# Optimization experiments

Measured on AMD Instinct MI355X. Metric: run time of the kernel, lower is better.

The kernel has to match this reference:

```python
import jax, jax.numpy as jnp
import numpy as np

HIDDEN = 2048
NUM_HEADS = 16
NUM_KV_HEADS = 16
QK_NOPE = 128
QK_ROPE = 64
HEAD_DIM = QK_NOPE + QK_ROPE  # 192
V_HEAD = 128
KV_LORA = 512
Q_LORA = 1536
EPS = 1e-6


def rmsnorm(x, w):
    var = jnp.mean(x * x, axis=-1, keepdims=True)
    return x * jax.lax.rsqrt(var + EPS) * w


def setup_inputs() -> dict:
    key = jax.random.key(0)
    ks = jax.random.split(key, 8)
    s = lambda fan_in: 1.0 / np.sqrt(fan_in)
    return {
        "hidden_states": jax.random.normal(ks[0], (2, 2048, HIDDEN), jnp.float32),
        # weights stored as [in, out] so forward is x @ W
        "q_a_w": jax.random.normal(ks[1], (HIDDEN, Q_LORA), jnp.float32) * s(HIDDEN),
        "q_a_ln_w": jnp.ones((Q_LORA,), jnp.float32),
        "q_b_w": jax.random.normal(ks[2], (Q_LORA, NUM_HEADS * HEAD_DIM), jnp.float32) * s(Q_LORA),
        "kv_a_w": jax.random.normal(ks[3], (HIDDEN, KV_LORA + NUM_KV_HEADS * QK_ROPE), jnp.float32) * s(HIDDEN),
        "kv_a_ln_w": jnp.ones((KV_LORA,), jnp.float32),
        "kv_b_w": jax.random.normal(ks[4], (KV_LORA, NUM_KV_HEADS * (QK_NOPE + V_HEAD)), jnp.float32) * s(KV_LORA),
        "o_w": jax.random.normal(ks[5], (NUM_HEADS * V_HEAD, HIDDEN), jnp.float32) * s(NUM_HEADS * V_HEAD),
    }


def reference(hidden_states, q_a_w, q_a_ln_w, q_b_w, kv_a_w, kv_a_ln_w, kv_b_w, o_w):
    B, T, _ = hidden_states.shape
    # Q path: low-rank down-proj -> RMSNorm -> up-proj
    q = rmsnorm(hidden_states @ q_a_w, q_a_ln_w) @ q_b_w
    q = q.reshape(B, T, NUM_HEADS, HEAD_DIM)  # [B,T,H,192]

    # KV path: joint down-proj producing latent + rope slice
    kv_raw = hidden_states @ kv_a_w
    kv_latent = rmsnorm(kv_raw[..., :KV_LORA], kv_a_ln_w)
    k_rope = kv_raw[..., KV_LORA:].reshape(B, T, NUM_KV_HEADS, QK_ROPE)
    kv = (kv_latent @ kv_b_w).reshape(B, T, NUM_KV_HEADS, QK_NOPE + V_HEAD)
    k_nope = kv[..., :QK_NOPE]
    v = kv[..., QK_NOPE:]  # [B,T,Hkv,128]

    # NOTE: the original forward computes RoPE cos/sin but never applies the
    # rotation; q_rope/k_rope are used as-is (faithfully reproduced here).
    k = jnp.concatenate([k_nope, k_rope], axis=-1)  # [B,T,Hkv,192]
    # num_kv_groups == 1, so no repeat_interleave needed

    scale = 1.0 / jnp.sqrt(jnp.float32(HEAD_DIM))
    scores = jnp.einsum("bqhd,bkhd->bhqk", q, k) * scale  # [B,H,T,T]
    causal = jnp.tril(jnp.ones((T, T), bool))
    scores = jnp.where(causal, scores, jnp.finfo(scores.dtype).min)
    probs = jax.nn.softmax(scores, axis=-1)
    attn = jnp.einsum("bhqk,bkhd->bqhd", probs, v)  # [B,T,H,128]
    attn = attn.reshape(B, T, NUM_HEADS * V_HEAD)
    return attn @ o_w
```

## Files before the change

### kernel.cpp

```cpp
#include <hip/hip_runtime.h>
#include <cstdint>
#include <cstddef>

typedef unsigned short u16;
typedef short short8 __attribute__((ext_vector_type(8)));
typedef float f32x4 __attribute__((ext_vector_type(4)));

#define B_   2
#define T_   2048
#define H_   16
#define HID_ 2048
#define DQK_ 192
#define DV_  128
#define AW_  3072

__device__ __forceinline__ float bf2f(u16 u) {
  unsigned int v = ((unsigned int)u) << 16;
  return __builtin_bit_cast(float, v);
}
__device__ __forceinline__ u16 f2bf(float f) {
  unsigned int u = __builtin_bit_cast(unsigned int, f);
  u += 0x7fff + ((u >> 16) & 1);
  return (u16)(u >> 16);
}
__device__ __forceinline__ void load_lds16(const void* g, void* l) {
  __builtin_amdgcn_global_load_lds((const __attribute__((address_space(1))) void*)g,
                                   (__attribute__((address_space(3))) void*)l, 16, 0, 0);
}

__global__ __launch_bounds__(256) void cast_f32_bf16(const float* __restrict__ x,
                                                     u16* __restrict__ y) {
  size_t i = ((size_t)blockIdx.x * 256 + threadIdx.x) * 8;
  float4 a = *(const float4*)&x[i];
  float4 b = *(const float4*)&x[i + 4];
  u16 r[8];
  r[0] = f2bf(a.x); r[1] = f2bf(a.y); r[2] = f2bf(a.z); r[3] = f2bf(a.w);
  r[4] = f2bf(b.x); r[5] = f2bf(b.y); r[6] = f2bf(b.z); r[7] = f2bf(b.w);
  *(uint4*)&y[i] = *(const uint4*)&r[0];
}

__global__ __launch_bounds__(256) void transpose_cast_k(const float* __restrict__ W,
                                                        u16* __restrict__ Wt,
                                                        int K, int N) {
  __shared__ u16 tile[32][33];
  int n0 = blockIdx.x * 32, k0 = blockIdx.y * 32;
  int tx = threadIdx.x & 31, ty = threadIdx.x >> 5;
#pragma unroll
  for (int i = 0; i < 32; i += 8)
    tile[ty + i][tx] = f2bf(W[(size_t)(k0 + ty + i) * N + n0 + tx]);
  __syncthreads();
#pragma unroll
  for (int i = 0; i < 32; i += 8)
    Wt[(size_t)(n0 + ty + i) * K + k0 + tx] = tile[tx][ty + i];
}

__global__ __launch_bounds__(256) void rmsnorm_k(const u16* __restrict__ in, int in_stride,
                                                 int L, const float* __restrict__ w,
                                                 u16* __restrict__ out, int out_stride) {
  int row = blockIdx.x;
  const u16* x = in + (size_t)row * in_stride;
  float ss = 0.f;
  for (int i = threadIdx.x * 8; i < L; i += 2048) {
    uint4 v = *(const uint4*)&x[i];
    const u16* p = (const u16*)&v;
#pragma unroll
    for (int e = 0; e < 8; ++e) { float f = bf2f(p[e]); ss += f * f; }
  }
#pragma unroll
  for (int m = 32; m >= 1; m >>= 1) ss += __shfl_xor(ss, m);
  __shared__ float red[4];
  if ((threadIdx.x & 63) == 0) red[threadIdx.x >> 6] = ss;
  __syncthreads();
  ss = red[0] + red[1] + red[2] + red[3];
  float inv = rsqrtf(ss / (float)L + 1e-6f);
  u16* o = out + (size_t)row * out_stride;
  for (int i = threadIdx.x * 8; i < L; i += 2048) {
    uint4 v = *(const uint4*)&x[i];
    const u16* p = (const u16*)&v;
    u16 r8[8];
#pragma unroll
    for (int e = 0; e < 8; ++e) r8[e] = f2bf(bf2f(p[e]) * inv * w[i + e]);
    *(uint4*)&o[i] = *(const uint4*)&r8[0];
  }
}

template <int EPI>
__global__ __launch_bounds__(256) void gemm_bt(const u16* __restrict__ A,
                                               const u16* __restrict__ Bt,
                                               void* __restrict__ Cout,
                                               int M, int N, int K) {
  __shared__ u16 As[3][128 * 32];
  __shared__ u16 Bs[3][128 * 32];
  const int nbx = N >> 7;
  const int bx = blockIdx.x % nbx, by = blockIdx.x / nbx;
  const int m0 = by << 7, n0 = bx << 7;
  const int tid = threadIdx.x, w = tid >> 6, lane = tid & 63;
  const int wr = w >> 1, wc = w & 1;
  const int llo = lane & 15, lhi = lane >> 4;
  f32x4 acc[4][4] = {};

  const int c0 = tid, c1 = tid + 256;
  const int ar0 = c0 >> 2, s0_ = c0 & 3;
  const int ar1 = c1 >> 2, s1_ = c1 & 3;
  const u16* Asrc0 = A + (size_t)(m0 + ar0) * K + (s0_ ^ ((ar0 >> 1) & 3)) * 8;
  const u16* Asrc1 = A + (size_t)(m0 + ar1) * K + (s1_ ^ ((ar1 >> 1) & 3)) * 8;
  const u16* Bsrc0 = Bt + (size_t)(n0 + ar0) * K + (s0_ ^ ((ar0 >> 1) & 3)) * 8;
  const u16* Bsrc1 = Bt + (size_t)(n0 + ar1) * K + (s1_ ^ ((ar1 >> 1) & 3)) * 8;

  int aoff[4], boff[4];
#pragma unroll
  for (int i = 0; i < 4; ++i) {
    int rowa = wr * 64 + i * 16 + llo;
    aoff[i] = (rowa * 4 + (lhi ^ ((rowa >> 1) & 3))) * 8;
    int rowb = wc * 64 + i * 16 + llo;
    boff[i] = (rowb * 4 + (lhi ^ ((rowb >> 1) & 3))) * 8;
  }

#define STAGE_KT(kt, buf)                                   \
  do {                                                      \
    int k0_ = (kt) << 5;                                    \
    load_lds16(Asrc0 + k0_, &As[(buf)][c0 * 8]);            \
    load_lds16(Asrc1 + k0_, &As[(buf)][c1 * 8]);            \
    load_lds16(Bsrc0 + k0_, &Bs[(buf)][c0 * 8]);            \
    load_lds16(Bsrc1 + k0_, &Bs[(buf)][c1 * 8]);            \
  } while (0)

  const int NT = K >> 5;
  STAGE_KT(0, 0);
  STAGE_KT(1, 1);
  asm volatile("s_waitcnt vmcnt(4)" ::: "memory");
  __builtin_amdgcn_s_barrier();

  int cur = 0, nxt = 2;
  for (int kt = 0; kt < NT; ++kt) {
    if (kt + 2 < NT) STAGE_KT(kt + 2, nxt);
    short8 af[4], bfr[4];
#pragma unroll
    for (int i = 0; i < 4; ++i) af[i] = *(const short8*)&As[cur][aoff[i]];
#pragma unroll
    for (int j = 0; j < 4; ++j) bfr[j] = *(const short8*)&Bs[cur][boff[j]];
    __builtin_amdgcn_s_setprio(1);
#pragma unroll
    for (int i = 0; i < 4; ++i)
#pragma unroll
      for (int j = 0; j < 4; ++j)
        acc[i][j] = __builtin_amdgcn_mfma_f32_16x16x32_bf16(af[i], bfr[j], acc[i][j], 0, 0, 0);
    __builtin_amdgcn_s_setprio(0);
    if (kt + 2 < NT) asm volatile("s_waitcnt vmcnt(4)" ::: "memory");
    else             asm volatile("s_waitcnt vmcnt(0)" ::: "memory");
    __builtin_amdgcn_s_barrier();
    cur = (cur == 2) ? 0 : cur + 1;
    nxt = (nxt == 2) ? 0 : nxt + 1;
  }
#undef STAGE_KT

  if constexpr (EPI == 0) {
    float* C = (float*)Cout;
#pragma unroll
    for (int i = 0; i < 4; ++i)
#pragma unroll
      for (int j = 0; j < 4; ++j)
#pragma unroll
        for (int r = 0; r < 4; ++r)
          C[(size_t)(m0 + wr * 64 + i * 16 + lhi * 4 + r) * N + (n0 + wc * 64 + j * 16 + llo)] =
              acc[i][j][r];
  } else {
    const float scale = (EPI == 3) ? 0.10412163f : 1.0f;
    u16* C = (u16*)Cout;
#pragma unroll
    for (int i = 0; i < 4; ++i)
#pragma unroll
      for (int j = 0; j < 4; ++j)
#pragma unroll
        for (int r = 0; r < 4; ++r)
          C[(size_t)(m0 + wr * 64 + i * 16 + lhi * 4 + r) * N + (n0 + wc * 64 + j * 16 + llo)] =
              f2bf(acc[i][j][r] * scale);
  }
}

__global__ __launch_bounds__(256) void pack_vt_k(const u16* __restrict__ kv, u16* __restrict__ Vt) {
  __shared__ u16 tile[64][136];
  const int nt = T_ / 64;
  int t0 = (blockIdx.x % nt) * 64;
  int bh = blockIdx.x / nt;
  int b = bh >> 4, h = bh & 15;
  int row = threadIdx.x >> 4;
  int ck = threadIdx.x & 15;
#pragma unroll
  for (int i = 0; i < 64; i += 16) {
    uint4 v = *(const uint4*)&kv[((size_t)(b * T_) + t0 + row + i) * 4096 + h * 256 + 128 + ck * 8];
    *(uint4*)&tile[row + i][ck * 8] = v;
  }
  __syncthreads();
  int d = threadIdx.x >> 1;
  int th = (threadIdx.x & 1) * 32;
  u16 tmp[32];
#pragma unroll
  for (int e = 0; e < 32; ++e) tmp[e] = tile[th + e][d];
#pragma unroll
  for (int e = 0; e < 32; e += 8)
    *(uint4*)&Vt[((size_t)bh * 128 + d) * T_ + t0 + th + e] = *(const uint4*)&tmp[e];
}

__global__ __launch_bounds__(256, 2) void attn_k(const u16* __restrict__ q,
                                                 const u16* __restrict__ kv,
                                                 const u16* __restrict__ kvraw,
                                                 const u16* __restrict__ Vt,
                                                 u16* __restrict__ att) {
  constexpr int KLD = 192, VLD = 64, PLD = 64;
  __shared__ u16 Ks[2][64 * KLD];
  __shared__ u16 Vs[128 * VLD];
  __shared__ u16 Ps[64 * PLD];
  const int p = (int)blockIdx.x;
  const int xcd = p & 7, j = p >> 3;
  const int bh = xcd * 4 + (j & 3);
  const int pr = j >> 2;
  const int b = bh >> 4, h = bh & 15;
  const int bT = b * T_;
  const int tid = threadIdx.x, w = tid >> 6, lane = tid & 63;
  const int llo = lane & 15, lhi = lane >> 4;
  const u16* Vb = Vt + (size_t)bh * DV_ * T_;

  const u16* kbase[6]; int kstr[6];
#pragma unroll
  for (int ii = 0; ii < 6; ++ii) {
    int c = ii * 256 + tid;
    int rr = c / 24, chk = c - rr * 24;
    int sc = chk ^ (rr & 7);
    if (sc < 16) { kbase[ii] = kv + (size_t)(bT + rr) * 4096 + h * 256 + sc * 8; kstr[ii] = 4096; }
    else { kbase[ii] = kvraw + (size_t)(bT + rr) * AW_ + 2048 + h * 64 + (sc - 16) * 8; kstr[ii] = AW_; }
  }
  int voff[4];
#pragma unroll
  for (int ii = 0; ii < 4; ++ii) {
    int c = ii * 256 + tid;
    int rr = c >> 3, chk = c & 7;
    voff[ii] = rr * T_ + (chk ^ (rr & 7)) * 8;
  }

#pragma unroll
  for (int pass = 0; pass < 2; ++pass) {
    const int qt = pass == 0 ? 31 - pr : pr;
    const int q0 = qt * 64;
    const int rbase = q0 + w * 16;
    short8 qf[6];
#pragma unroll
    for (int kk = 0; kk < 6; ++kk)
      qf[kk] = *(const short8*)&q[(size_t)(bT + rbase + llo) * AW_ + h * DQK_ + kk * 32 + lhi * 8];
    f32x4 oacc[8] = {};
    float m_r[4], l_r[4];
#pragma unroll
    for (int r = 0; r < 4; ++r) { m_r[r] = -1e30f; l_r[r] = 0.f; }

#pragma unroll
    for (int ii = 0; ii < 6; ++ii)
      load_lds16(kbase[ii], &Ks[0][(ii * 256 + tid) * 8]);
    asm volatile("s_waitcnt vmcnt(0)" ::: "memory");
    __builtin_amdgcn_s_barrier();
    __builtin_amdgcn_sched_barrier(0);

    const int nkt = qt + 1;
    int cur = 0;
    for (int kt = 0; kt < nkt; ++kt) {
      const int k0 = kt * 64;
      const bool hasNext = (kt + 1 < nkt);
#pragma unroll
      for (int ii = 0; ii < 4; ++ii)
        load_lds16(Vb + k0 + voff[ii], &Vs[(ii * 256 + tid) * 8]);
      if (hasNext) {
        u16* kd = Ks[cur ^ 1];
#pragma unroll
        for (int ii = 0; ii < 6; ++ii)
          load_lds16(kbase[ii] + (size_t)(k0 + 64) * kstr[ii], &kd[(ii * 256 + tid) * 8]);
      }
      const u16* kbuf = Ks[cur];
      f32x4 s[4] = {};
      __builtin_amdgcn_s_setprio(1);
#pragma unroll
      for (int kk = 0; kk < 6; ++kk) {
        const int col = kk * 32 + lhi * 8;
        short8 kf[4];
#pragma unroll
        for (int j2 = 0; j2 < 4; ++j2) {
          const int row = j2 * 16 + llo;
          kf[j2] = *(const short8*)&kbuf[row * KLD + (col ^ ((row & 7) << 3))];
        }
#pragma unroll
        for (int j2 = 0; j2 < 4; ++j2)
          s[j2] = __builtin_amdgcn_mfma_f32_16x16x32_bf16(qf[kk], kf[j2], s[j2], 0, 0, 0);
      }
      __builtin_amdgcn_s_setprio(0);
      const bool needMask = (k0 + 63 > rbase);
#pragma unroll
      for (int r = 0; r < 4; ++r) {
        const int qrow = rbase + lhi * 4 + r;
        float sv[4];
#pragma unroll
        for (int j2 = 0; j2 < 4; ++j2) {
          float x = s[j2][r];
          if (needMask) { int kcol = k0 + j2 * 16 + llo; x = (kcol <= qrow) ? x : -1e30f; }
          sv[j2] = x;
        }
        float mx4 = fmaxf(fmaxf(sv[0], sv[1]), fmaxf(sv[2], sv[3]));
        if (!__all(mx4 - m_r[r] <= 8.f)) {
          float mx = mx4;
#pragma unroll
          for (int mk = 1; mk < 16; mk <<= 1) mx = fmaxf(mx, __shfl_xor(mx, mk));
          float mnew = fmaxf(m_r[r], mx);
          float alpha = exp2f(m_r[r] - mnew);
          m_r[r] = mnew;
          l_r[r] *= alpha;
#pragma unroll
          for (int jo = 0; jo < 8; ++jo) oacc[jo][r] *= alpha;
        }
        float rs = 0.f;
        const int prow = w * 16 + lhi * 4 + r;
#pragma unroll
        for (int j2 = 0; j2 < 4; ++j2) {
          float p2 = exp2f(sv[j2] - m_r[r]);
          rs += p2;
          int pcol = j2 * 16 + llo;
          Ps[prow * PLD + (pcol ^ ((prow & 7) << 3))] = f2bf(p2);
        }
        l_r[r] += rs;
      }
      if (hasNext) asm volatile("s_waitcnt vmcnt(6)" ::: "memory");
      else         asm volatile("s_waitcnt vmcnt(0)" ::: "memory");
      __builtin_amdgcn_s_barrier();
      __builtin_amdgcn_sched_barrier(0);
      __builtin_amdgcn_s_setprio(1);
#pragma unroll
      for (int kk2 = 0; kk2 < 2; ++kk2) {
        const int prow = w * 16 + llo;
        const int pcol = kk2 * 32 + lhi * 8;
        short8 pf = *(const short8*)&Ps[prow * PLD + (pcol ^ ((prow & 7) << 3))];
#pragma unroll
        for (int jo = 0; jo < 8; ++jo) {
          const int vrow = jo * 16 + llo;
          short8 vf = *(const short8*)&Vs[vrow * VLD + (pcol ^ ((vrow & 7) << 3))];
          oacc[jo] = __builtin_amdgcn_mfma_f32_16x16x32_bf16(pf, vf, oacc[jo], 0, 0, 0);
        }
      }
      __builtin_amdgcn_s_setprio(0);
      asm volatile("s_waitcnt vmcnt(0)" ::: "memory");
      __builtin_amdgcn_s_barrier();
      __builtin_amdgcn_sched_barrier(0);
      cur ^= 1;
    }
#pragma unroll
    for (int r = 0; r < 4; ++r) {
      float lr = l_r[r];
#pragma unroll
      for (int mk = 1; mk < 16; mk <<= 1) lr += __shfl_xor(lr, mk);
      const int qrow = rbase + lhi * 4 + r;
      const float linv = 1.f / lr;
#pragma unroll
      for (int jo = 0; jo < 8; ++jo)
        att[((size_t)bT + qrow) * (H_ * DV_) + h * DV_ + jo * 16 + llo] =
            f2bf(oacc[jo][r] * linv);
    }
  }
}

extern "C" void kernel_launch(void* const* d_in, const int* in_sizes, int n_in,
                              void* d_out, int out_size, void* d_ws, size_t ws_size,
                              hipStream_t stream) {
  const float* hs      = (const float*)d_in[0];
  const float* q_a_w   = (const float*)d_in[1];
  const float* q_a_ln  = (const float*)d_in[2];
  const float* q_b_w   = (const float*)d_in[3];
  const float* kv_a_w  = (const float*)d_in[4];
  const float* kv_a_ln = (const float*)d_in[5];
  const float* kv_b_w  = (const float*)d_in[6];
  const float* o_w     = (const float*)d_in[7];
  float* out = (float*)d_out;
  char* ws = (char*)d_ws;

  u16* hid  = (u16*)(ws + 0);
  u16* wt   = (u16*)(ws + 16777216);
  u16* qa   = (u16*)(ws + 29360128);
  u16* qan  = (u16*)(ws + 54525952);
  u16* qout = (u16*)(ws + 67108864);
  u16* att  = (u16*)(ws + 92274688);
  u16* kv   = (u16*)(ws + 109051904);
  u16* Vt   = (u16*)(ws + 142606336);

  cast_f32_bf16<<<4096, 256, 0, stream>>>(hs, hid);

  transpose_cast_k<<<dim3(1536 / 32, 2048 / 32), 256, 0, stream>>>(q_a_w, wt, 2048, 1536);
  transpose_cast_k<<<dim3(1536 / 32, 2048 / 32), 256, 0, stream>>>(kv_a_w, wt + (size_t)1536 * 2048, 2048, 1536);
  gemm_bt<1><<<(3072 / 128) * (4096 / 128), 256, 0, stream>>>(hid, wt, qa, 4096, 3072, 2048);

  rmsnorm_k<<<4096, 256, 0, stream>>>(qa, AW_, 1536, q_a_ln, qan, 1536);

  transpose_cast_k<<<dim3(3072 / 32, 1536 / 32), 256, 0, stream>>>(q_b_w, wt, 1536, 3072);
  gemm_bt<3><<<(3072 / 128) * (4096 / 128), 256, 0, stream>>>(qan, wt, qout, 4096, 3072, 1536);

  rmsnorm_k<<<4096, 256, 0, stream>>>(qa + 1536, AW_, 512, kv_a_ln, qan, 512);

  transpose_cast_k<<<dim3(4096 / 32, 512 / 32), 256, 0, stream>>>(kv_b_w, wt, 512, 4096);
  gemm_bt<1><<<(4096 / 128) * (4096 / 128), 256, 0, stream>>>(qan, wt, kv, 4096, 4096, 512);

  pack_vt_k<<<1024, 256, 0, stream>>>(kv, Vt);

  attn_k<<<512, 256, 0, stream>>>(qout, kv, qa, Vt, att);

  transpose_cast_k<<<dim3(2048 / 32, 2048 / 32), 256, 0, stream>>>(o_w, wt, 2048, 2048);
  gemm_bt<0><<<(2048 / 128) * (4096 / 128), 256, 0, stream>>>(att, wt, out, 4096, 2048, 2048);
}
```

Before: 336.4 us.

## Use 32-key tiles, double-buffer V, and one query tile per block

The attention kernel now gives each block a single 64-row query tile, launched as 1024 blocks in heaviest-first order, instead of pairing a heavy and a light tile per block. K tiles shrink to 32 keys and V is double-buffered alongside K, which removes one barrier per iteration. LDS use drops enough to allow three blocks per CU. The aim is better overlap of loads with MFMA work and higher occupancy. The cost is more loop iterations with less MFMA work each, and losing the explicit causal load pairing.

```diff
diff --git a/kernel.cpp b/kernel.cpp
--- a/kernel.cpp
+++ b/kernel.cpp
@@ -202,163 +202,159 @@
     *(uint4*)&Vt[((size_t)bh * 128 + d) * T_ + t0 + th + e] = *(const uint4*)&tmp[e];
 }
 
-__global__ __launch_bounds__(256, 2) void attn_k(const u16* __restrict__ q,
+__global__ __launch_bounds__(256, 3) void attn_k(const u16* __restrict__ q,
                                                  const u16* __restrict__ kv,
                                                  const u16* __restrict__ kvraw,
                                                  const u16* __restrict__ Vt,
                                                  u16* __restrict__ att) {
-  constexpr int KLD = 192, VLD = 64, PLD = 64;
-  __shared__ u16 Ks[2][64 * KLD];
-  __shared__ u16 Vs[128 * VLD];
+  constexpr int KLD = 192;
+  constexpr int VLD = 32;
+  constexpr int PLD = 32;
+  __shared__ u16 Ks[2][32 * KLD];
+  __shared__ u16 Vs[2][128 * VLD];
   __shared__ u16 Ps[64 * PLD];
   const int p = (int)blockIdx.x;
   const int xcd = p & 7, j = p >> 3;
   const int bh = xcd * 4 + (j & 3);
-  const int pr = j >> 2;
+  const int qt = 31 - (j >> 2);
   const int b = bh >> 4, h = bh & 15;
   const int bT = b * T_;
+  const int q0 = qt * 64;
   const int tid = threadIdx.x, w = tid >> 6, lane = tid & 63;
   const int llo = lane & 15, lhi = lane >> 4;
+  const int rbase = q0 + w * 16;
   const u16* Vb = Vt + (size_t)bh * DV_ * T_;
 
-  const u16* kbase[6]; int kstr[6];
-#pragma unroll
-  for (int ii = 0; ii < 6; ++ii) {
+  const u16* kbase[3]; int kstr[3];
+#pragma unroll
+  for (int ii = 0; ii < 3; ++ii) {
     int c = ii * 256 + tid;
     int rr = c / 24, chk = c - rr * 24;
     int sc = chk ^ (rr & 7);
     if (sc < 16) { kbase[ii] = kv + (size_t)(bT + rr) * 4096 + h * 256 + sc * 8; kstr[ii] = 4096; }
     else { kbase[ii] = kvraw + (size_t)(bT + rr) * AW_ + 2048 + h * 64 + (sc - 16) * 8; kstr[ii] = AW_; }
   }
-  int voff[4];
-#pragma unroll
-  for (int ii = 0; ii < 4; ++ii) {
+  const u16* vsrc[2];
+#pragma unroll
+  for (int ii = 0; ii < 2; ++ii) {
     int c = ii * 256 + tid;
-    int rr = c >> 3, chk = c & 7;
-    voff[ii] = rr * T_ + (chk ^ (rr & 7)) * 8;
-  }
-
-#pragma unroll
-  for (int pass = 0; pass < 2; ++pass) {
-    const int qt = pass == 0 ? 31 - pr : pr;
-    const int q0 = qt * 64;
-    const int rbase = q0 + w * 16;
-    short8 qf[6];
-#pragma unroll
-    for (int kk = 0; kk < 6; ++kk)
-      qf[kk] = *(const short8*)&q[(size_t)(bT + rbase + llo) * AW_ + h * DQK_ + kk * 32 + lhi * 8];
-    f32x4 oacc[8] = {};
-    float m_r[4], l_r[4];
-#pragma unroll
-    for (int r = 0; r < 4; ++r) { m_r[r] = -1e30f; l_r[r] = 0.f; }
-
-#pragma unroll
-    for (int ii = 0; ii < 6; ++ii)
-      load_lds16(kbase[ii], &Ks[0][(ii * 256 + tid) * 8]);
+    int rr = c >> 2, sl = c & 3;
+    vsrc[ii] = Vb + (size_t)rr * T_ + (sl ^ (rr & 3)) * 8;
+  }
+
+  short8 qf[6];
+#pragma unroll
+  for (int kk = 0; kk < 6; ++kk)
+    qf[kk] = *(const short8*)&q[(size_t)(bT + rbase + llo) * AW_ + h * DQK_ + kk * 32 + lhi * 8];
+  f32x4 oacc[8] = {};
+  float m_r[4], l_r[4];
+#pragma unroll
+  for (int r = 0; r < 4; ++r) { m_r[r] = -1e30f; l_r[r] = 0.f; }
+
+#pragma unroll
+  for (int ii = 0; ii < 3; ++ii)
+    load_lds16(kbase[ii], &Ks[0][(ii * 256 + tid) * 8]);
+#pragma unroll
+  for (int ii = 0; ii < 2; ++ii)
+    load_lds16(vsrc[ii], &Vs[0][(ii * 256 + tid) * 8]);
+  asm volatile("s_waitcnt vmcnt(0)" ::: "memory");
+  __builtin_amdgcn_s_barrier();
+  __builtin_amdgcn_sched_barrier(0);
+
+  const int nkt = 2 * qt + 2;
+  int cur = 0;
+  for (int kt = 0; kt < nkt; ++kt) {
+    const int k0 = kt * 32;
+    if (kt + 1 < nkt) {
+      u16* kd = Ks[cur ^ 1];
+      u16* vd = Vs[cur ^ 1];
+#pragma unroll
+      for (int ii = 0; ii < 3; ++ii)
+        load_lds16(kbase[ii] + (size_t)(k0 + 32) * kstr[ii], &kd[(ii * 256 + tid) * 8]);
+#pragma unroll
+      for (int ii = 0; ii < 2; ++ii)
+        load_lds16(vsrc[ii] + k0 + 32, &vd[(ii * 256 + tid) * 8]);
+    }
+    const u16* kbuf = Ks[cur];
+    f32x4 s[2] = {};
+    __builtin_amdgcn_s_setprio(1);
+#pragma unroll
+    for (int kk = 0; kk < 6; ++kk) {
+      const int col = kk * 32 + lhi * 8;
+      short8 kf[2];
+#pragma unroll
+      for (int j2 = 0; j2 < 2; ++j2) {
+        const int row = j2 * 16 + llo;
+        kf[j2] = *(const short8*)&kbuf[row * KLD + (col ^ ((row & 7) << 3))];
+      }
+#pragma unroll
+      for (int j2 = 0; j2 < 2; ++j2)
+        s[j2] = __builtin_amdgcn_mfma_f32_16x16x32_bf16(qf[kk], kf[j2], s[j2], 0, 0, 0);
+    }
+    __builtin_amdgcn_s_setprio(0);
+    const bool needMask = (k0 + 31 > rbase);
+#pragma unroll
+    for (int r = 0; r < 4; ++r) {
+      const int qrow = rbase + lhi * 4 + r;
+      float sv[2];
+#pragma unroll
+      for (int j2 = 0; j2 < 2; ++j2) {
+        float x = s[j2][r];
+        if (needMask) { int kcol = k0 + j2 * 16 + llo; x = (kcol <= qrow) ? x : -1e30f; }
+        sv[j2] = x;
+      }
+      float mx2 = fmaxf(sv[0], sv[1]);
+      if (!__all(mx2 - m_r[r] <= 8.f)) {
+        float mx = mx2;
+#pragma unroll
+        for (int mk = 1; mk < 16; mk <<= 1) mx = fmaxf(mx, __shfl_xor(mx, mk));
+        float mnew = fmaxf(m_r[r], mx);
+        float alpha = exp2f(m_r[r] - mnew);
+        m_r[r] = mnew;
+        l_r[r] *= alpha;
+#pragma unroll
+        for (int jo = 0; jo < 8; ++jo) oacc[jo][r] *= alpha;
+      }
+      const int prow = w * 16 + lhi * 4 + r;
+      float rs = 0.f;
+#pragma unroll
+      for (int j2 = 0; j2 < 2; ++j2) {
+        float pv = exp2f(sv[j2] - m_r[r]);
+        rs += pv;
+        int pcol = j2 * 16 + llo;
+        int slot = pcol >> 3;
+        Ps[prow * PLD + ((slot ^ (prow & 3)) * 8) + (pcol & 7)] = f2bf(pv);
+      }
+      l_r[r] += rs;
+    }
+    __builtin_amdgcn_s_setprio(1);
+    {
+      const int prow = w * 16 + llo;
+      short8 pf = *(const short8*)&Ps[prow * PLD + ((lhi ^ (prow & 3)) * 8)];
+#pragma unroll
+      for (int jo = 0; jo < 8; ++jo) {
+        const int vrow = jo * 16 + llo;
+        short8 vf = *(const short8*)&Vs[cur][vrow * VLD + ((lhi ^ (vrow & 3)) * 8)];
+        oacc[jo] = __builtin_amdgcn_mfma_f32_16x16x32_bf16(pf, vf, oacc[jo], 0, 0, 0);
+      }
+    }
+    __builtin_amdgcn_s_setprio(0);
     asm volatile("s_waitcnt vmcnt(0)" ::: "memory");
     __builtin_amdgcn_s_barrier();
     __builtin_amdgcn_sched_barrier(0);
-
-    const int nkt = qt + 1;
-    int cur = 0;
-    for (int kt = 0; kt < nkt; ++kt) {
-      const int k0 = kt * 64;
-      const bool hasNext = (kt + 1 < nkt);
-#pragma unroll
-      for (int ii = 0; ii < 4; ++ii)
-        load_lds16(Vb + k0 + voff[ii], &Vs[(ii * 256 + tid) * 8]);
-      if (hasNext) {
-        u16* kd = Ks[cur ^ 1];
-#pragma unroll
-        for (int ii = 0; ii < 6; ++ii)
-          load_lds16(kbase[ii] + (size_t)(k0 + 64) * kstr[ii], &kd[(ii * 256 + tid) * 8]);
-      }
-      const u16* kbuf = Ks[cur];
-      f32x4 s[4] = {};
-      __builtin_amdgcn_s_setprio(1);
-#pragma unroll
-      for (int kk = 0; kk < 6; ++kk) {
-        const int col = kk * 32 + lhi * 8;
-        short8 kf[4];
-#pragma unroll
-        for (int j2 = 0; j2 < 4; ++j2) {
-          const int row = j2 * 16 + llo;
-          kf[j2] = *(const short8*)&kbuf[row * KLD + (col ^ ((row & 7) << 3))];
-        }
-#pragma unroll
-        for (int j2 = 0; j2 < 4; ++j2)
-          s[j2] = __builtin_amdgcn_mfma_f32_16x16x32_bf16(qf[kk], kf[j2], s[j2], 0, 0, 0);
-      }
-      __builtin_amdgcn_s_setprio(0);
-      const bool needMask = (k0 + 63 > rbase);
-#pragma unroll
-      for (int r = 0; r < 4; ++r) {
-        const int qrow = rbase + lhi * 4 + r;
-        float sv[4];
-#pragma unroll
-        for (int j2 = 0; j2 < 4; ++j2) {
-          float x = s[j2][r];
-          if (needMask) { int kcol = k0 + j2 * 16 + llo; x = (kcol <= qrow) ? x : -1e30f; }
-          sv[j2] = x;
-        }
-        float mx4 = fmaxf(fmaxf(sv[0], sv[1]), fmaxf(sv[2], sv[3]));
-        if (!__all(mx4 - m_r[r] <= 8.f)) {
-          float mx = mx4;
-#pragma unroll
-          for (int mk = 1; mk < 16; mk <<= 1) mx = fmaxf(mx, __shfl_xor(mx, mk));
-          float mnew = fmaxf(m_r[r], mx);
-          float alpha = exp2f(m_r[r] - mnew);
-          m_r[r] = mnew;
-          l_r[r] *= alpha;
-#pragma unroll
-          for (int jo = 0; jo < 8; ++jo) oacc[jo][r] *= alpha;
-        }
-        float rs = 0.f;
-        const int prow = w * 16 + lhi * 4 + r;
-#pragma unroll
-        for (int j2 = 0; j2 < 4; ++j2) {
-          float p2 = exp2f(sv[j2] - m_r[r]);
-          rs += p2;
-          int pcol = j2 * 16 + llo;
-          Ps[prow * PLD + (pcol ^ ((prow & 7) << 3))] = f2bf(p2);
-        }
-        l_r[r] += rs;
-      }
-      if (hasNext) asm volatile("s_waitcnt vmcnt(6)" ::: "memory");
-      else         asm volatile("s_waitcnt vmcnt(0)" ::: "memory");
-      __builtin_amdgcn_s_barrier();
-      __builtin_amdgcn_sched_barrier(0);
-      __builtin_amdgcn_s_setprio(1);
-#pragma unroll
-      for (int kk2 = 0; kk2 < 2; ++kk2) {
-        const int prow = w * 16 + llo;
-        const int pcol = kk2 * 32 + lhi * 8;
-        short8 pf = *(const short8*)&Ps[prow * PLD + (pcol ^ ((prow & 7) << 3))];
-#pragma unroll
-        for (int jo = 0; jo < 8; ++jo) {
-          const int vrow = jo * 16 + llo;
-          short8 vf = *(const short8*)&Vs[vrow * VLD + (pcol ^ ((vrow & 7) << 3))];
-          oacc[jo] = __builtin_amdgcn_mfma_f32_16x16x32_bf16(pf, vf, oacc[jo], 0, 0, 0);
-        }
-      }
-      __builtin_amdgcn_s_setprio(0);
-      asm volatile("s_waitcnt vmcnt(0)" ::: "memory");
-      __builtin_amdgcn_s_barrier();
-      __builtin_amdgcn_sched_barrier(0);
-      cur ^= 1;
-    }
-#pragma unroll
-    for (int r = 0; r < 4; ++r) {
-      float lr = l_r[r];
-#pragma unroll
-      for (int mk = 1; mk < 16; mk <<= 1) lr += __shfl_xor(lr, mk);
-      const int qrow = rbase + lhi * 4 + r;
-      const float linv = 1.f / lr;
-#pragma unroll
-      for (int jo = 0; jo < 8; ++jo)
-        att[((size_t)bT + qrow) * (H_ * DV_) + h * DV_ + jo * 16 + llo] =
-            f2bf(oacc[jo][r] * linv);
-    }
+    cur ^= 1;
+  }
+#pragma unroll
+  for (int r = 0; r < 4; ++r) {
+    float lr = l_r[r];
+#pragma unroll
+    for (int mk = 1; mk < 16; mk <<= 1) lr += __shfl_xor(lr, mk);
+    const int qrow = rbase + lhi * 4 + r;
+    const float linv = 1.f / lr;
+#pragma unroll
+    for (int jo = 0; jo < 8; ++jo)
+      att[((size_t)bT + qrow) * (H_ * DV_) + h * DV_ + jo * 16 + llo] =
+          f2bf(oacc[jo][r] * linv);
   }
 }
 
@@ -403,7 +399,7 @@
 
   pack_vt_k<<<1024, 256, 0, stream>>>(kv, Vt);
 
-  attn_k<<<512, 256, 0, stream>>>(qout, kv, qa, Vt, att);
+  attn_k<<<1024, 256, 0, stream>>>(qout, kv, qa, Vt, att);
 
   transpose_cast_k<<<dim3(2048 / 32, 2048 / 32), 256, 0, stream>>>(o_w, wt, 2048, 2048);
   gemm_bt<0><<<(2048 / 128) * (4096 / 128), 256, 0, stream>>>(att, wt, out, 4096, 2048, 2048);
```

After: 439.3 us. +30.6%, slower.

## Add 256x256 eight-wave GEMM with staged LDS prefetch for projection GEMMs

Applied to the files above, without the earlier changes.

Introduces a new bf16 GEMM kernel using 256x256 output tiles, 512 threads, K-step 64, double-buffered LDS with swizzled async loads interleaved between four MFMA quadrant phases, and s_setprio around the MFMA bursts. It replaces the 128x128 GEMM for the Q-down/KV-down, Q-up and KV-up projections to raise arithmetic intensity and overlap global loads with compute. The larger tiles mean fewer blocks (192 to 256), which can underfill a 256-CU device and leave some CUs idle. Large LDS use (128KB) and register pressure also limit occupancy.

```diff
diff --git a/kernel.cpp b/kernel.cpp
--- a/kernel.cpp
+++ b/kernel.cpp
@@ -82,6 +82,134 @@
     for (int e = 0; e < 8; ++e) r8[e] = f2bf(bf2f(p[e]) * inv * w[i + e]);
     *(uint4*)&o[i] = *(const uint4*)&r8[0];
   }
+}
+
+template <int EPI>
+__global__ __launch_bounds__(512) void gemm256(const u16* __restrict__ A,
+                                               const u16* __restrict__ Bt,
+                                               void* __restrict__ Cout,
+                                               int M, int N, int K) {
+  __shared__ u16 As[2][256 * 64];
+  __shared__ u16 Bs[2][256 * 64];
+  const int nbx = N >> 8;
+  const int bx = blockIdx.x % nbx, by = blockIdx.x / nbx;
+  const int m0 = by << 8, n0 = bx << 8;
+  const int tid = threadIdx.x, w = tid >> 6, lane = tid & 63;
+  const int wm = w >> 2, wn = w & 3;
+  const int llo = lane & 15, lhi = lane >> 4;
+  f32x4 acc[8][4] = {};
+
+  const u16* srcp[8];
+  int dsto[8];
+#pragma unroll
+  for (int jl = 0; jl < 2; ++jl) {
+    int c = jl * 512 + tid;
+    int i = c >> 3, sl = c & 7;
+    { int r = ((i >> 6) << 7) + (i & 63);
+      srcp[jl] = A + (size_t)(m0 + r) * K + ((sl ^ (r & 7)) << 3);
+      dsto[jl] = (r * 8 + sl) * 8; }
+    { int r = ((i >> 5) << 6) + (i & 31);
+      srcp[2 + jl] = Bt + (size_t)(n0 + r) * K + ((sl ^ (r & 7)) << 3);
+      dsto[2 + jl] = (r * 8 + sl) * 8; }
+    { int r = ((i >> 5) << 6) + 32 + (i & 31);
+      srcp[4 + jl] = Bt + (size_t)(n0 + r) * K + ((sl ^ (r & 7)) << 3);
+      dsto[4 + jl] = (r * 8 + sl) * 8; }
+    { int r = ((i >> 6) << 7) + 64 + (i & 63);
+      srcp[6 + jl] = A + (size_t)(m0 + r) * K + ((sl ^ (r & 7)) << 3);
+      dsto[6 + jl] = (r * 8 + sl) * 8; }
+  }
+#define STG(j, kt, buf)                                                        \
+  load_lds16(srcp[j] + (size_t)(kt) * 64,                                      \
+             ((j) < 2 || (j) >= 6) ? &As[(buf)][dsto[j]] : &Bs[(buf)][dsto[j]])
+
+  auto rdA = [&](int buf, int mi, int ks) {
+    int r = wm * 128 + mi * 16 + llo;
+    return *(const short8*)&As[buf][r * 64 + (((ks * 4 + lhi) ^ (r & 7)) << 3)];
+  };
+  auto rdB = [&](int buf, int nj, int ks) {
+    int r = wn * 64 + nj * 16 + llo;
+    return *(const short8*)&Bs[buf][r * 64 + (((ks * 4 + lhi) ^ (r & 7)) << 3)];
+  };
+
+  const int NT = K >> 6;
+#pragma unroll
+  for (int j = 0; j < 8; ++j) STG(j, 0, 0);
+
+  short8 af[4][2], bf[2][2];
+  for (int kt = 0; kt < NT; ++kt) {
+    const int cur = kt & 1, nxt = cur ^ 1;
+    const bool hn = (kt + 1 < NT);
+    asm volatile("s_waitcnt vmcnt(4)" ::: "memory");
+    __builtin_amdgcn_s_barrier();
+#pragma unroll
+    for (int mi = 0; mi < 4; ++mi) { af[mi][0] = rdA(cur, mi, 0); af[mi][1] = rdA(cur, mi, 1); }
+#pragma unroll
+    for (int nj = 0; nj < 2; ++nj) { bf[nj][0] = rdB(cur, nj, 0); bf[nj][1] = rdB(cur, nj, 1); }
+    if (hn) { STG(0, kt + 1, nxt); STG(1, kt + 1, nxt); }
+    __builtin_amdgcn_s_setprio(1);
+#pragma unroll
+    for (int mi = 0; mi < 4; ++mi)
+#pragma unroll
+      for (int nj = 0; nj < 2; ++nj)
+#pragma unroll
+        for (int ks = 0; ks < 2; ++ks)
+          acc[mi][nj] = __builtin_amdgcn_mfma_f32_16x16x32_bf16(af[mi][ks], bf[nj][ks], acc[mi][nj], 0, 0, 0);
+    __builtin_amdgcn_s_setprio(0);
+    if (hn) asm volatile("s_waitcnt vmcnt(4)" ::: "memory");
+    else    asm volatile("s_waitcnt vmcnt(2)" ::: "memory");
+    __builtin_amdgcn_s_barrier();
+#pragma unroll
+    for (int nj = 0; nj < 2; ++nj) { bf[nj][0] = rdB(cur, 2 + nj, 0); bf[nj][1] = rdB(cur, 2 + nj, 1); }
+    if (hn) { STG(2, kt + 1, nxt); STG(3, kt + 1, nxt); }
+    __builtin_amdgcn_s_setprio(1);
+#pragma unroll
+    for (int mi = 0; mi < 4; ++mi)
+#pragma unroll
+      for (int nj = 0; nj < 2; ++nj)
+#pragma unroll
+        for (int ks = 0; ks < 2; ++ks)
+          acc[mi][2 + nj] = __builtin_amdgcn_mfma_f32_16x16x32_bf16(af[mi][ks], bf[nj][ks], acc[mi][2 + nj], 0, 0, 0);
+    __builtin_amdgcn_s_setprio(0);
+    if (hn) asm volatile("s_waitcnt vmcnt(4)" ::: "memory");
+    else    asm volatile("s_waitcnt vmcnt(0)" ::: "memory");
+    __builtin_amdgcn_s_barrier();
+#pragma unroll
+    for (int mi = 0; mi < 4; ++mi) { af[mi][0] = rdA(cur, 4 + mi, 0); af[mi][1] = rdA(cur, 4 + mi, 1); }
+    if (hn) { STG(4, kt + 1, nxt); STG(5, kt + 1, nxt); }
+    __builtin_amdgcn_s_setprio(1);
+#pragma unroll
+    for (int mi = 0; mi < 4; ++mi)
+#pragma unroll
+      for (int nj = 0; nj < 2; ++nj)
+#pragma unroll
+        for (int ks = 0; ks < 2; ++ks)
+          acc[4 + mi][2 + nj] = __builtin_amdgcn_mfma_f32_16x16x32_bf16(af[mi][ks], bf[nj][ks], acc[4 + mi][2 + nj], 0, 0, 0);
+    __builtin_amdgcn_s_setprio(0);
+#pragma unroll
+    for (int nj = 0; nj < 2; ++nj) { bf[nj][0] = rdB(cur, nj, 0); bf[nj][1] = rdB(cur, nj, 1); }
+    if (hn) { STG(6, kt + 1, nxt); STG(7, kt + 1, nxt); }
+    __builtin_amdgcn_s_setprio(1);
+#pragma unroll
+    for (int mi = 0; mi < 4; ++mi)
+#pragma unroll
+      for (int nj = 0; nj < 2; ++nj)
+#pragma unroll
+        for (int ks = 0; ks < 2; ++ks)
+          acc[4 + mi][nj] = __builtin_amdgcn_mfma_f32_16x16x32_bf16(af[mi][ks], bf[nj][ks], acc[4 + mi][nj], 0, 0, 0);
+    __builtin_amdgcn_s_setprio(0);
+  }
+#undef STG
+
+  const float scale = (EPI == 3) ? 0.10412163f : 1.0f;
+  u16* C = (u16*)Cout;
+#pragma unroll
+  for (int mi = 0; mi < 8; ++mi)
+#pragma unroll
+    for (int nj = 0; nj < 4; ++nj)
+#pragma unroll
+      for (int r = 0; r < 4; ++r)
+        C[(size_t)(m0 + wm * 128 + mi * 16 + lhi * 4 + r) * N + (n0 + wn * 64 + nj * 16 + llo)] =
+            f2bf(acc[mi][nj][r] * scale);
 }
 
 template <int EPI>
@@ -389,17 +517,17 @@
 
   transpose_cast_k<<<dim3(1536 / 32, 2048 / 32), 256, 0, stream>>>(q_a_w, wt, 2048, 1536);
   transpose_cast_k<<<dim3(1536 / 32, 2048 / 32), 256, 0, stream>>>(kv_a_w, wt + (size_t)1536 * 2048, 2048, 1536);
-  gemm_bt<1><<<(3072 / 128) * (4096 / 128), 256, 0, stream>>>(hid, wt, qa, 4096, 3072, 2048);
+  gemm256<1><<<(3072 / 256) * (4096 / 256), 512, 0, stream>>>(hid, wt, qa, 4096, 3072, 2048);
 
   rmsnorm_k<<<4096, 256, 0, stream>>>(qa, AW_, 1536, q_a_ln, qan, 1536);
 
   transpose_cast_k<<<dim3(3072 / 32, 1536 / 32), 256, 0, stream>>>(q_b_w, wt, 1536, 3072);
-  gemm_bt<3><<<(3072 / 128) * (4096 / 128), 256, 0, stream>>>(qan, wt, qout, 4096, 3072, 1536);
+  gemm256<3><<<(3072 / 256) * (4096 / 256), 512, 0, stream>>>(qan, wt, qout, 4096, 3072, 1536);
 
   rmsnorm_k<<<4096, 256, 0, stream>>>(qa + 1536, AW_, 512, kv_a_ln, qan, 512);
 
   transpose_cast_k<<<dim3(4096 / 32, 512 / 32), 256, 0, stream>>>(kv_b_w, wt, 512, 4096);
-  gemm_bt<1><<<(4096 / 128) * (4096 / 128), 256, 0, stream>>>(qan, wt, kv, 4096, 4096, 512);
+  gemm256<1><<<(4096 / 256) * (4096 / 256), 512, 0, stream>>>(qan, wt, kv, 4096, 4096, 512);
 
   pack_vt_k<<<1024, 256, 0, stream>>>(kv, Vt);
 
```

Measured after the change: 320.7 us. 4.7% less time.
